# Kernel optimization log

Measured on AMD Instinct MI355X. Metric: run time of the kernel, lower is better.

Reference implementation:

```python
import jax, jax.numpy as jnp
import numpy as np

EPS = 1e-5  # torch BatchNorm1d default eps


def setup_inputs() -> dict:
    key = jax.random.key(0)
    ks = jax.random.split(key, 8)
    B, H, D, DO = 8192, 8, 512, 256
    return {
        "x_concepts_encoded": jax.random.normal(ks[0], (B, H, D), dtype=jnp.float32),
        "relevance_weights": jax.random.uniform(ks[1], (B, H), dtype=jnp.float32),
        "bn_gamma": jax.random.uniform(ks[2], (D,), dtype=jnp.float32) + 0.5,
        "bn_beta": jax.random.normal(ks[3], (D,), dtype=jnp.float32) * 0.1,
        "bn_mean": jax.random.normal(ks[4], (D,), dtype=jnp.float32) * 0.1,
        "bn_var": jax.random.uniform(ks[5], (D,), dtype=jnp.float32) + 0.5,
        "W": jax.random.normal(ks[6], (DO, D), dtype=jnp.float32) / np.sqrt(D),
        "b": jax.random.normal(ks[7], (DO,), dtype=jnp.float32) * 0.01,
    }


def reference(x_concepts_encoded, relevance_weights, bn_gamma, bn_beta, bn_mean, bn_var, W, b):
    B, H = relevance_weights.shape
    x = x_concepts_encoded.reshape(B * H, -1)            # [B*H, D]
    # BatchNorm1d (inference: running stats) fused as scale/shift
    inv = bn_gamma * jax.lax.rsqrt(bn_var + EPS)
    h = x * inv + (bn_beta - bn_mean * inv)              # [B*H, D]
    # Swish
    h = h * jax.nn.sigmoid(h)
    # Linear
    out = h @ W.T + b                                    # [B*H, DO]
    # relevance-weighted sum over heads
    out = jnp.einsum('bhd,bh->bd', out.reshape(B, H, -1), relevance_weights)
    return out
```

## Files before the change

kernel.cpp:

```cpp
#include <hip/hip_runtime.h>
#include <hip/hip_bf16.h>

#define NB 8192
#define NH 8
#define ND 512
#define NO 256
#define ROWS 32
#define TPB 512

typedef __attribute__((ext_vector_type(8))) short short8;
typedef __attribute__((ext_vector_type(4))) float f32x4;

__device__ __align__(16) ushort g_wb[NO * ND];

__device__ __forceinline__ ushort f2bf(float f) {
    union { float f; unsigned u; } v; v.f = f;
    unsigned u = v.u;
    unsigned r = u + 0x7FFFu + ((u >> 16) & 1u);
    return (ushort)(r >> 16);
}

__global__ __launch_bounds__(256) void wcvt_kernel(const float* __restrict__ W) {
    int i = (blockIdx.x * 256 + threadIdx.x) * 4;
    float4 w = *(const float4*)(W + i);
    ushort4 o;
    o.x = f2bf(w.x); o.y = f2bf(w.y); o.z = f2bf(w.z); o.w = f2bf(w.w);
    *(ushort4*)(g_wb + i) = o;
}

__device__ __forceinline__ float swishf(float h) {
    return h * __builtin_amdgcn_rcpf(1.0f + __expf(-h));
}

__global__ __launch_bounds__(TPB) void fused_kernel(
    const float* __restrict__ x, const float* __restrict__ rw,
    const float* __restrict__ gamma, const float* __restrict__ beta,
    const float* __restrict__ mean, const float* __restrict__ var,
    const float* __restrict__ bias, float* __restrict__ out)
{
    __shared__ __align__(16) ushort yl[ROWS * ND];
    __shared__ float rwl[ROWS * NH];

    const int tid = threadIdx.x;
    const int b0  = blockIdx.x * ROWS;
    const int d4  = tid & 127;
    const int rh  = tid >> 7;
    const int d   = d4 * 4;

    if (tid < 64)
        ((float4*)rwl)[tid] = ((const float4*)(rw + (size_t)b0 * NH))[tid];

    float4 g4 = *(const float4*)(gamma + d);
    float4 v4 = *(const float4*)(var   + d);
    float4 be = *(const float4*)(beta  + d);
    float4 me = *(const float4*)(mean  + d);
    const float ix = g4.x * rsqrtf(v4.x + 1e-5f);
    const float iy = g4.y * rsqrtf(v4.y + 1e-5f);
    const float iz = g4.z * rsqrtf(v4.z + 1e-5f);
    const float iw = g4.w * rsqrtf(v4.w + 1e-5f);
    const float ox = be.x - me.x * ix;
    const float oy = be.y - me.y * iy;
    const float oz = be.z - me.z * iz;
    const float ow = be.w - me.w * iw;

    __syncthreads();

    #pragma unroll
    for (int it = 0; it < 8; ++it) {
        const int rr = rh + it * 4;
        const float* xr = x + (size_t)(b0 + rr) * (NH * ND) + d;
        const float4 w0 = ((const float4*)(rwl + rr * NH))[0];
        const float4 w1 = ((const float4*)(rwl + rr * NH))[1];
        const float whv[NH] = {w0.x, w0.y, w0.z, w0.w, w1.x, w1.y, w1.z, w1.w};

        float ax = 0.f, ay = 0.f, az = 0.f, aw = 0.f;
        #pragma unroll
        for (int h = 0; h < NH; ++h) {
            float4 xa = *(const float4*)(xr + h * ND);
            const float wh = whv[h];
            ax += wh * swishf(xa.x * ix + ox);
            ay += wh * swishf(xa.y * iy + oy);
            az += wh * swishf(xa.z * iz + oz);
            aw += wh * swishf(xa.w * iw + ow);
        }
        const int addr = rr * 1024 + ((d * 2) ^ ((rr & 7) << 4));
        ushort4 o;
        o.x = f2bf(ax); o.y = f2bf(ay); o.z = f2bf(az); o.w = f2bf(aw);
        *(ushort4*)((char*)yl + addr) = o;
    }
    __syncthreads();

    const int lane = tid & 63;
    const int wv   = tid >> 6;
    const int n0   = wv * 32;
    const int lr   = lane & 15;
    const int lk   = (lane >> 4) * 8;

    f32x4 acc00 = {0.f,0.f,0.f,0.f};
    f32x4 acc01 = {0.f,0.f,0.f,0.f};
    f32x4 acc10 = {0.f,0.f,0.f,0.f};
    f32x4 acc11 = {0.f,0.f,0.f,0.f};

    const char* ylb0 = (const char*)yl + lr * 1024;
    const char* ylb1 = (const char*)yl + (lr + 16) * 1024;
    const int swz = (lr & 7) << 4;

    #pragma unroll
    for (int ks = 0; ks < 16; ++ks) {
        const int k0 = ks * 32;
        const int kb = (k0 + lk) * 2;
        short8 a0 = *(const short8*)(ylb0 + (kb ^ swz));
        short8 a1 = *(const short8*)(ylb1 + (kb ^ swz));
        const ushort* wp = g_wb + (size_t)(n0 + lr) * ND + k0 + lk;
        short8 bf0 = *(const short8*)(wp);
        short8 bf1 = *(const short8*)(wp + 16 * ND);
        acc00 = __builtin_amdgcn_mfma_f32_16x16x32_bf16(a0, bf0, acc00, 0, 0, 0);
        acc01 = __builtin_amdgcn_mfma_f32_16x16x32_bf16(a0, bf1, acc01, 0, 0, 0);
        acc10 = __builtin_amdgcn_mfma_f32_16x16x32_bf16(a1, bf0, acc10, 0, 0, 0);
        acc11 = __builtin_amdgcn_mfma_f32_16x16x32_bf16(a1, bf1, acc11, 0, 0, 0);
    }

    const int rbase = (lane >> 4) * 4;
    float sw0[4], sw1[4];
    #pragma unroll
    for (int q = 0; q < 4; ++q) {
        const float* rp0 = rwl + (rbase + q) * NH;
        const float* rp1 = rwl + (16 + rbase + q) * NH;
        sw0[q] = ((rp0[0]+rp0[1]) + (rp0[2]+rp0[3])) + ((rp0[4]+rp0[5]) + (rp0[6]+rp0[7]));
        sw1[q] = ((rp1[0]+rp1[1]) + (rp1[2]+rp1[3])) + ((rp1[4]+rp1[5]) + (rp1[6]+rp1[7]));
    }
    f32x4 accs0[2] = {acc00, acc01};
    f32x4 accs1[2] = {acc10, acc11};
    #pragma unroll
    for (int nf = 0; nf < 2; ++nf) {
        const int col = n0 + nf * 16 + lr;
        const float bn = bias[col];
        #pragma unroll
        for (int q = 0; q < 4; ++q) {
            const int r = rbase + q;
            out[(size_t)(b0 + r) * NO + col]      = accs0[nf][q] + bn * sw0[q];
            out[(size_t)(b0 + 16 + r) * NO + col] = accs1[nf][q] + bn * sw1[q];
        }
    }
}

extern "C" void kernel_launch(void* const* d_in, const int* in_sizes, int n_in,
                              void* d_out, int out_size, void* d_ws, size_t ws_size,
                              hipStream_t stream) {
    const float* x     = (const float*)d_in[0];
    const float* rw    = (const float*)d_in[1];
    const float* gamma = (const float*)d_in[2];
    const float* beta  = (const float*)d_in[3];
    const float* mean  = (const float*)d_in[4];
    const float* var   = (const float*)d_in[5];
    const float* W     = (const float*)d_in[6];
    const float* bias  = (const float*)d_in[7];
    float* out = (float*)d_out;

    hipLaunchKernelGGL(wcvt_kernel, dim3((NO * ND) / 1024), dim3(256), 0, stream, W);
    hipLaunchKernelGGL(fused_kernel, dim3(NB / ROWS), dim3(TPB), 0, stream,
                       x, rw, gamma, beta, mean, var, bias, out);
}
```

Before: 38.87 us.

## Fuse W bf16 conversion into main kernel and preload W fragments into registers

Drops the separate weight-conversion kernel. Each wave now loads its fp32 W slice directly, converts it to bf16 and keeps all 16 k-step B fragments in registers, loaded before the barrier so the loads overlap the swish stage. The MFMA loop then reads only from LDS. In exchange every block re-reads and re-converts fp32 W (double the bytes of the bf16 copy), register pressure rises (launch bounds now request 2 blocks), and one kernel launch is removed.

```diff
diff --git a/kernel.cpp b/kernel.cpp
--- a/kernel.cpp
+++ b/kernel.cpp
@@ -11,8 +11,6 @@
 typedef __attribute__((ext_vector_type(8))) short short8;
 typedef __attribute__((ext_vector_type(4))) float f32x4;
 
-__device__ __align__(16) ushort g_wb[NO * ND];
-
 __device__ __forceinline__ ushort f2bf(float f) {
     union { float f; unsigned u; } v; v.f = f;
     unsigned u = v.u;
@@ -20,23 +18,25 @@
     return (ushort)(r >> 16);
 }
 
-__global__ __launch_bounds__(256) void wcvt_kernel(const float* __restrict__ W) {
-    int i = (blockIdx.x * 256 + threadIdx.x) * 4;
-    float4 w = *(const float4*)(W + i);
-    ushort4 o;
-    o.x = f2bf(w.x); o.y = f2bf(w.y); o.z = f2bf(w.z); o.w = f2bf(w.w);
-    *(ushort4*)(g_wb + i) = o;
-}
-
 __device__ __forceinline__ float swishf(float h) {
     return h * __builtin_amdgcn_rcpf(1.0f + __expf(-h));
 }
 
-__global__ __launch_bounds__(TPB) void fused_kernel(
+__device__ __forceinline__ short8 pack8(float4 a, float4 b) {
+    short8 r;
+    r[0] = (short)f2bf(a.x); r[1] = (short)f2bf(a.y);
+    r[2] = (short)f2bf(a.z); r[3] = (short)f2bf(a.w);
+    r[4] = (short)f2bf(b.x); r[5] = (short)f2bf(b.y);
+    r[6] = (short)f2bf(b.z); r[7] = (short)f2bf(b.w);
+    return r;
+}
+
+__global__ __launch_bounds__(TPB, 2) void fused_kernel(
     const float* __restrict__ x, const float* __restrict__ rw,
     const float* __restrict__ gamma, const float* __restrict__ beta,
     const float* __restrict__ mean, const float* __restrict__ var,
-    const float* __restrict__ bias, float* __restrict__ out)
+    const float* __restrict__ W, const float* __restrict__ bias,
+    float* __restrict__ out)
 {
     __shared__ __align__(16) ushort yl[ROWS * ND];
     __shared__ float rwl[ROWS * NH];
@@ -46,6 +46,12 @@
     const int d4  = tid & 127;
     const int rh  = tid >> 7;
     const int d   = d4 * 4;
+
+    const int lane = tid & 63;
+    const int wv   = tid >> 6;
+    const int n0   = wv * 32;
+    const int lr   = lane & 15;
+    const int lk   = (lane >> 4) * 8;
 
     if (tid < 64)
         ((float4*)rwl)[tid] = ((const float4*)(rw + (size_t)b0 * NH))[tid];
@@ -88,13 +94,23 @@
         o.x = f2bf(ax); o.y = f2bf(ay); o.z = f2bf(az); o.w = f2bf(aw);
         *(ushort4*)((char*)yl + addr) = o;
     }
+
+    short8 wb0[16], wb1[16];
+    {
+        const float* wp0 = W + (size_t)(n0 + lr) * ND + lk;
+        const float* wp1 = wp0 + 16 * ND;
+        #pragma unroll
+        for (int ks = 0; ks < 16; ++ks) {
+            float4 a0 = *(const float4*)(wp0 + ks * 32);
+            float4 a1 = *(const float4*)(wp0 + ks * 32 + 4);
+            float4 b0 = *(const float4*)(wp1 + ks * 32);
+            float4 b1 = *(const float4*)(wp1 + ks * 32 + 4);
+            wb0[ks] = pack8(a0, a1);
+            wb1[ks] = pack8(b0, b1);
+        }
+    }
+    __builtin_amdgcn_sched_barrier(0);
     __syncthreads();
-
-    const int lane = tid & 63;
-    const int wv   = tid >> 6;
-    const int n0   = wv * 32;
-    const int lr   = lane & 15;
-    const int lk   = (lane >> 4) * 8;
 
     f32x4 acc00 = {0.f,0.f,0.f,0.f};
     f32x4 acc01 = {0.f,0.f,0.f,0.f};
@@ -107,17 +123,13 @@
 
     #pragma unroll
     for (int ks = 0; ks < 16; ++ks) {
-        const int k0 = ks * 32;
-        const int kb = (k0 + lk) * 2;
+        const int kb = (ks * 32 + lk) * 2;
         short8 a0 = *(const short8*)(ylb0 + (kb ^ swz));
         short8 a1 = *(const short8*)(ylb1 + (kb ^ swz));
-        const ushort* wp = g_wb + (size_t)(n0 + lr) * ND + k0 + lk;
-        short8 bf0 = *(const short8*)(wp);
-        short8 bf1 = *(const short8*)(wp + 16 * ND);
-        acc00 = __builtin_amdgcn_mfma_f32_16x16x32_bf16(a0, bf0, acc00, 0, 0, 0);
-        acc01 = __builtin_amdgcn_mfma_f32_16x16x32_bf16(a0, bf1, acc01, 0, 0, 0);
-        acc10 = __builtin_amdgcn_mfma_f32_16x16x32_bf16(a1, bf0, acc10, 0, 0, 0);
-        acc11 = __builtin_amdgcn_mfma_f32_16x16x32_bf16(a1, bf1, acc11, 0, 0, 0);
+        acc00 = __builtin_amdgcn_mfma_f32_16x16x32_bf16(a0, wb0[ks], acc00, 0, 0, 0);
+        acc01 = __builtin_amdgcn_mfma_f32_16x16x32_bf16(a0, wb1[ks], acc01, 0, 0, 0);
+        acc10 = __builtin_amdgcn_mfma_f32_16x16x32_bf16(a1, wb0[ks], acc10, 0, 0, 0);
+        acc11 = __builtin_amdgcn_mfma_f32_16x16x32_bf16(a1, wb1[ks], acc11, 0, 0, 0);
     }
 
     const int rbase = (lane >> 4) * 4;
@@ -157,7 +169,6 @@
     const float* bias  = (const float*)d_in[7];
     float* out = (float*)d_out;
 
-    hipLaunchKernelGGL(wcvt_kernel, dim3((NO * ND) / 1024), dim3(256), 0, stream, W);
     hipLaunchKernelGGL(fused_kernel, dim3(NB / ROWS), dim3(TPB), 0, stream,
-                       x, rw, gamma, beta, mean, var, bias, out);
+                       x, rw, gamma, beta, mean, var, W, bias, out);
 }
```

Result: slower. 48.22 us (+24.0%).

## Double block size to 1024 threads and prefetch weight fragments before barrier

Applied to the files above, without the earlier changes.

Raises the block to 1024 threads (16 waves) so each wave computes a 32x16 output tile instead of 32x32, and each thread handles 4 rows of the swish/head-reduction phase instead of 8. It also issues the first four bf16 weight-fragment loads from global memory before the barrier and keeps a 4-deep register ring of weight loads inside the MFMA loop, so global-load latency overlaps the barrier and the MFMAs. The aim is more waves in flight for latency hiding and less exposed weight-load latency. The cost is more threads contending for the block's LDS, and the weight rows are now loaded by twice as many waves per block.

```diff
diff --git a/kernel.cpp b/kernel.cpp
--- a/kernel.cpp
+++ b/kernel.cpp
@@ -6,7 +6,7 @@
 #define ND 512
 #define NO 256
 #define ROWS 32
-#define TPB 512
+#define TPB 1024
 
 typedef __attribute__((ext_vector_type(8))) short short8;
 typedef __attribute__((ext_vector_type(4))) float f32x4;
@@ -47,6 +47,12 @@
     const int rh  = tid >> 7;
     const int d   = d4 * 4;
 
+    const int lane = tid & 63;
+    const int wv   = tid >> 6;
+    const int n0   = wv * 16;
+    const int lr   = lane & 15;
+    const int lk   = (lane >> 4) * 8;
+
     if (tid < 64)
         ((float4*)rwl)[tid] = ((const float4*)(rw + (size_t)b0 * NH))[tid];
 
@@ -66,8 +72,8 @@
     __syncthreads();
 
     #pragma unroll
-    for (int it = 0; it < 8; ++it) {
-        const int rr = rh + it * 4;
+    for (int it = 0; it < 4; ++it) {
+        const int rr = rh + it * 8;
         const float* xr = x + (size_t)(b0 + rr) * (NH * ND) + d;
         const float4 w0 = ((const float4*)(rwl + rr * NH))[0];
         const float4 w1 = ((const float4*)(rwl + rr * NH))[1];
@@ -88,18 +94,17 @@
         o.x = f2bf(ax); o.y = f2bf(ay); o.z = f2bf(az); o.w = f2bf(aw);
         *(ushort4*)((char*)yl + addr) = o;
     }
+
+    const ushort* wp = g_wb + (size_t)(n0 + lr) * ND + lk;
+    short8 rb[4];
+    #pragma unroll
+    for (int p = 0; p < 4; ++p)
+        rb[p] = *(const short8*)(wp + p * 32);
+    __builtin_amdgcn_sched_barrier(0);
     __syncthreads();
 
-    const int lane = tid & 63;
-    const int wv   = tid >> 6;
-    const int n0   = wv * 32;
-    const int lr   = lane & 15;
-    const int lk   = (lane >> 4) * 8;
-
-    f32x4 acc00 = {0.f,0.f,0.f,0.f};
-    f32x4 acc01 = {0.f,0.f,0.f,0.f};
-    f32x4 acc10 = {0.f,0.f,0.f,0.f};
-    f32x4 acc11 = {0.f,0.f,0.f,0.f};
+    f32x4 acc0 = {0.f,0.f,0.f,0.f};
+    f32x4 acc1 = {0.f,0.f,0.f,0.f};
 
     const char* ylb0 = (const char*)yl + lr * 1024;
     const char* ylb1 = (const char*)yl + (lr + 16) * 1024;
@@ -107,17 +112,14 @@
 
     #pragma unroll
     for (int ks = 0; ks < 16; ++ks) {
-        const int k0 = ks * 32;
-        const int kb = (k0 + lk) * 2;
+        short8 b = rb[ks & 3];
+        if (ks + 4 < 16)
+            rb[ks & 3] = *(const short8*)(wp + (ks + 4) * 32);
+        const int kb = (ks * 32 + lk) * 2;
         short8 a0 = *(const short8*)(ylb0 + (kb ^ swz));
         short8 a1 = *(const short8*)(ylb1 + (kb ^ swz));
-        const ushort* wp = g_wb + (size_t)(n0 + lr) * ND + k0 + lk;
-        short8 bf0 = *(const short8*)(wp);
-        short8 bf1 = *(const short8*)(wp + 16 * ND);
-        acc00 = __builtin_amdgcn_mfma_f32_16x16x32_bf16(a0, bf0, acc00, 0, 0, 0);
-        acc01 = __builtin_amdgcn_mfma_f32_16x16x32_bf16(a0, bf1, acc01, 0, 0, 0);
-        acc10 = __builtin_amdgcn_mfma_f32_16x16x32_bf16(a1, bf0, acc10, 0, 0, 0);
-        acc11 = __builtin_amdgcn_mfma_f32_16x16x32_bf16(a1, bf1, acc11, 0, 0, 0);
+        acc0 = __builtin_amdgcn_mfma_f32_16x16x32_bf16(a0, b, acc0, 0, 0, 0);
+        acc1 = __builtin_amdgcn_mfma_f32_16x16x32_bf16(a1, b, acc1, 0, 0, 0);
     }
 
     const int rbase = (lane >> 4) * 4;
@@ -129,18 +131,13 @@
         sw0[q] = ((rp0[0]+rp0[1]) + (rp0[2]+rp0[3])) + ((rp0[4]+rp0[5]) + (rp0[6]+rp0[7]));
         sw1[q] = ((rp1[0]+rp1[1]) + (rp1[2]+rp1[3])) + ((rp1[4]+rp1[5]) + (rp1[6]+rp1[7]));
     }
-    f32x4 accs0[2] = {acc00, acc01};
-    f32x4 accs1[2] = {acc10, acc11};
+    const int col = n0 + lr;
+    const float bn = bias[col];
     #pragma unroll
-    for (int nf = 0; nf < 2; ++nf) {
-        const int col = n0 + nf * 16 + lr;
-        const float bn = bias[col];
-        #pragma unroll
-        for (int q = 0; q < 4; ++q) {
-            const int r = rbase + q;
-            out[(size_t)(b0 + r) * NO + col]      = accs0[nf][q] + bn * sw0[q];
-            out[(size_t)(b0 + 16 + r) * NO + col] = accs1[nf][q] + bn * sw1[q];
-        }
+    for (int q = 0; q < 4; ++q) {
+        const int r = rbase + q;
+        out[(size_t)(b0 + r) * NO + col]      = acc0[q] + bn * sw0[q];
+        out[(size_t)(b0 + 16 + r) * NO + col] = acc1[q] + bn * sw1[q];
     }
 }
 
```

Result: faster. 37.86 us, median of 2 (-2.6%).
